# Kernel optimization log

Hardware: AMD Instinct MI355X
Metric: run time of the kernel (lower is better)

Reference implementation:

```python
import jax, jax.numpy as jnp
import numpy as np

T, HID, H, KV, D = 2048, 2048, 16, 8, 128
EPS = 1e-6
THETA = 10000.0


def setup_inputs() -> dict:
    key = jax.random.key(0)
    ks = jax.random.split(key, 6)
    positions = jnp.arange(T, dtype=jnp.int64 if jax.config.jax_enable_x64 else jnp.int32)
    hidden_states = jax.random.normal(ks[0], (T, HID), dtype=jnp.float32)
    scale = 0.02
    Wq = jax.random.normal(ks[1], (HID, H * 2 * D), dtype=jnp.float32) * scale
    Wk = jax.random.normal(ks[2], (HID, KV * D), dtype=jnp.float32) * scale
    Wv = jax.random.normal(ks[3], (HID, KV * D), dtype=jnp.float32) * scale
    Wo = jax.random.normal(ks[4], (H * D, HID), dtype=jnp.float32) * scale
    q_norm_w = jnp.zeros((D,), dtype=jnp.float32)  # torch init: zeros, applied as (1+w)
    k_norm_w = jnp.zeros((D,), dtype=jnp.float32)
    return {"positions": positions, "hidden_states": hidden_states, "Wq": Wq,
            "Wk": Wk, "Wv": Wv, "Wo": Wo, "q_norm_w": q_norm_w, "k_norm_w": k_norm_w}


def _rms_norm(x, w):
    # fp32 RMSNorm with (1 + weight) scaling, per last dim
    xf = x.astype(jnp.float32)
    inv = jax.lax.rsqrt(jnp.mean(xf * xf, axis=-1, keepdims=True) + EPS)
    return (xf * inv * (1.0 + w.astype(jnp.float32))).astype(x.dtype)


def _rope(x, positions):
    # neox-style rotary over full head_dim; x: (T, heads, D)
    half = D // 2
    inv_freq = 1.0 / (THETA ** (jnp.arange(0, half, dtype=jnp.float32) / half))
    freqs = positions.astype(jnp.float32)[:, None] * inv_freq  # (T, half)
    cos = jnp.cos(freqs)[:, None, :]  # (T,1,half)
    sin = jnp.sin(freqs)[:, None, :]
    x1, x2 = x[..., :half], x[..., half:]
    return jnp.concatenate([x1 * cos - x2 * sin, x2 * cos + x1 * sin], axis=-1)


def reference(positions, hidden_states, Wq, Wk, Wv, Wo, q_norm_w, k_norm_w):
    scaling = D ** -0.5
    qg = (hidden_states @ Wq).reshape(T, H, 2 * D)
    q, gate = qg[..., :D], qg[..., D:]              # (T,H,D) each
    k = (hidden_states @ Wk).reshape(T, KV, D)
    v = (hidden_states @ Wv).reshape(T, KV, D)
    q = _rms_norm(q, q_norm_w)
    k = _rms_norm(k, k_norm_w)
    q = _rope(q, positions)
    k = _rope(k, positions)
    # GQA: repeat kv heads
    rep = H // KV
    k = jnp.repeat(k, rep, axis=1)                   # (T,H,D)
    v = jnp.repeat(v, rep, axis=1)
    scores = jnp.einsum('thd,shd->hts', q, k) * scaling  # (H,T,T)
    causal = positions[:, None] >= positions[None, :]     # (T,T)
    scores = jnp.where(causal[None], scores, jnp.finfo(scores.dtype).min)
    probs = jax.nn.softmax(scores, axis=-1)
    o = jnp.einsum('hts,shd->thd', probs, v).reshape(T, H * D)
    o = o * jax.nn.sigmoid(gate.reshape(T, H * D))
    return o @ Wo
```

## Files before the change

kernel.cpp:

```cpp
#include <hip/hip_runtime.h>
#include <stdint.h>
#include <math.h>

#define T_SEQ 2048
#define HID   2048
#define NH    16
#define NKV   8
#define DH    128

typedef __bf16 bf16x8 __attribute__((ext_vector_type(8)));
typedef float  f32x4  __attribute__((ext_vector_type(4)));

__device__ __forceinline__ ushort f2bf(float f) {
  uint32_t u = __float_as_uint(f);
  u += 0x7FFF + ((u >> 16) & 1);
  return (ushort)(u >> 16);
}
__device__ __forceinline__ float bf2f(ushort u) {
  return __uint_as_float(((uint32_t)u) << 16);
}
__device__ __forceinline__ void gld16(const void* g, void* l) {
  __builtin_amdgcn_global_load_lds(
      (const __attribute__((address_space(1))) uint32_t*)g,
      (__attribute__((address_space(3))) uint32_t*)l, 16, 0, 0);
}

__global__ __launch_bounds__(256) void prep_kernel(
    const float* __restrict__ hs, const float* __restrict__ Wq,
    const float* __restrict__ Wk, const float* __restrict__ Wv,
    const float* __restrict__ qnw, const float* __restrict__ knw,
    ushort* __restrict__ hs16, ushort* __restrict__ Wqt,
    ushort* __restrict__ Wkt, ushort* __restrict__ Wvt,
    float* __restrict__ bnd) {
  int bid = blockIdx.x;
  if (bid < 4096) {
    int i = (bid * 256 + threadIdx.x) * 4;
    float4 v = *(const float4*)(hs + i);
    ushort4 o = {f2bf(v.x), f2bf(v.y), f2bf(v.z), f2bf(v.w)};
    *(ushort4*)(hs16 + i) = o;
    return;
  }
  if (bid == 16384) {
    int t = threadIdx.x;
    if (t >= 128) return;
    float mq = fabsf(1.f + qnw[t]);
    float mk = fabsf(1.f + knw[t]);
#pragma unroll
    for (int off = 32; off >= 1; off >>= 1) {
      mq = fmaxf(mq, __shfl_xor(mq, off, 64));
      mk = fmaxf(mk, __shfl_xor(mk, off, 64));
    }
    __shared__ float s4[4];
    if ((t & 63) == 0) { s4[(t >> 6) * 2] = mq; s4[(t >> 6) * 2 + 1] = mk; }
    __syncthreads();
    if (t == 0) {
      float MQ = fmaxf(s4[0], s4[2]), MK = fmaxf(s4[1], s4[3]);
      bnd[0] = 16.3217f * MQ * MK * 1.02f + 0.1f;
    }
    return;
  }
  bid -= 4096;
  const float* src; ushort* dst; int N, bi, bj;
  if (bid < 8192)       { src = Wq; dst = Wqt; N = 4096; bj = bid & 127; bi = bid >> 7; }
  else if (bid < 10240) { bid -= 8192;  src = Wk; dst = Wkt; N = 1024; bj = bid & 31; bi = bid >> 5; }
  else                  { bid -= 10240; src = Wv; dst = Wvt; N = 1024; bj = bid & 31; bi = bid >> 5; }
  __shared__ float tile[32][33];
  int row = threadIdx.x >> 3, c4 = (threadIdx.x & 7) * 4;
  float4 v = *(const float4*)(src + (size_t)(bi * 32 + row) * N + bj * 32 + c4);
  tile[row][c4 + 0] = v.x; tile[row][c4 + 1] = v.y;
  tile[row][c4 + 2] = v.z; tile[row][c4 + 3] = v.w;
  __syncthreads();
  ushort4 o = {f2bf(tile[c4 + 0][row]), f2bf(tile[c4 + 1][row]),
               f2bf(tile[c4 + 2][row]), f2bf(tile[c4 + 3][row])};
  *(ushort4*)(dst + (size_t)(bj * 32 + row) * HID + bi * 32 + c4) = o;
}

__global__ __launch_bounds__(256) void prep_wo(const float* __restrict__ Wo,
                                               ushort* __restrict__ Wot) {
  int bid = blockIdx.x;
  int bj = bid & 63, bi = bid >> 6;
  __shared__ float tile[32][33];
  int row = threadIdx.x >> 3, c4 = (threadIdx.x & 7) * 4;
  float4 v = *(const float4*)(Wo + (size_t)(bi * 32 + row) * HID + bj * 32 + c4);
  tile[row][c4 + 0] = v.x; tile[row][c4 + 1] = v.y;
  tile[row][c4 + 2] = v.z; tile[row][c4 + 3] = v.w;
  __syncthreads();
  ushort4 o = {f2bf(tile[c4 + 0][row]), f2bf(tile[c4 + 1][row]),
               f2bf(tile[c4 + 2][row]), f2bf(tile[c4 + 3][row])};
  *(ushort4*)(Wot + (size_t)(bj * 32 + row) * HID + bi * 32 + c4) = o;
}

template <int OUT_BF16>
__device__ __forceinline__ void gemm_core(
    const ushort* __restrict__ A, const ushort* __restrict__ Bt,
    float* __restrict__ Cf, ushort* __restrict__ Cb, int N, int K,
    int m0, int n0, ushort* As, ushort* Bs) {
  const int tid = threadIdx.x, lane = tid & 63, w = tid >> 6;
  const int quad = lane >> 4, l15 = lane & 15;
  const int wm = (w >> 1) * 64, wn = (w & 1) * 64;
  f32x4 acc[4][4];
#pragma unroll
  for (int i = 0; i < 4; ++i)
#pragma unroll
    for (int j = 0; j < 4; ++j) acc[i][j] = (f32x4){0.f, 0.f, 0.f, 0.f};

  const int srow = tid >> 2, sch = tid & 3;
  for (int k0 = 0; k0 < K; k0 += 32) {
    __syncthreads();
#pragma unroll
    for (int p = 0; p < 2; ++p) {
      int row = p * 64 + srow;
      int gch = sch ^ ((row >> 1) & 3);
      gld16(A + (size_t)(m0 + row) * K + k0 + gch * 8,
            As + (p * 256 + w * 64) * 8);
      gld16(Bt + (size_t)(n0 + row) * K + k0 + gch * 8,
            Bs + (p * 256 + w * 64) * 8);
    }
    __syncthreads();
    bf16x8 af[4], bfr[4];
#pragma unroll
    for (int mi = 0; mi < 4; ++mi) {
      int row = wm + mi * 16 + l15;
      int pch = quad ^ ((row >> 1) & 3);
      af[mi] = *(const bf16x8*)(As + row * 32 + pch * 8);
    }
#pragma unroll
    for (int ni = 0; ni < 4; ++ni) {
      int row = wn + ni * 16 + l15;
      int pch = quad ^ ((row >> 1) & 3);
      bfr[ni] = *(const bf16x8*)(Bs + row * 32 + pch * 8);
    }
#pragma unroll
    for (int mi = 0; mi < 4; ++mi)
#pragma unroll
      for (int ni = 0; ni < 4; ++ni)
        acc[mi][ni] = __builtin_amdgcn_mfma_f32_16x16x32_bf16(
            af[mi], bfr[ni], acc[mi][ni], 0, 0, 0);
  }
#pragma unroll
  for (int mi = 0; mi < 4; ++mi)
#pragma unroll
    for (int ni = 0; ni < 4; ++ni)
#pragma unroll
      for (int r = 0; r < 4; ++r) {
        int row = m0 + wm + mi * 16 + quad * 4 + r;
        int col = n0 + wn + ni * 16 + l15;
        if (OUT_BF16) Cb[(size_t)row * N + col] = f2bf(acc[mi][ni][r]);
        else          Cf[(size_t)row * N + col] = acc[mi][ni][r];
      }
}

__global__ __launch_bounds__(256) void gemm_qkv(
    const ushort* __restrict__ hs16, const ushort* __restrict__ Wqt,
    const ushort* __restrict__ Wkt, const ushort* __restrict__ Wvt,
    ushort* __restrict__ qg16, ushort* __restrict__ kb16,
    ushort* __restrict__ v16t) {
  __shared__ ushort As[128 * 32];
  __shared__ ushort Bs[128 * 32];
  int b = blockIdx.x;
  if (b < 512) {
    gemm_core<1>(hs16, Wqt, nullptr, qg16, 4096, HID, (b >> 5) * 128,
                 (b & 31) * 128, As, Bs);
  } else if (b < 640) {
    int f = b - 512;
    gemm_core<1>(hs16, Wkt, nullptr, kb16, 1024, HID, (f >> 3) * 128,
                 (f & 7) * 128, As, Bs);
  } else {
    int f = b - 640;
    gemm_core<1>(Wvt, hs16, nullptr, v16t, 2048, HID, (f >> 4) * 128,
                 (f & 15) * 128, As, Bs);
  }
}

__global__ __launch_bounds__(256) void gemm_out(
    const ushort* __restrict__ ob16, const ushort* __restrict__ Wot,
    float* __restrict__ out) {
  __shared__ ushort As[128 * 32];
  __shared__ ushort Bs[128 * 32];
  int b = blockIdx.x;
  gemm_core<0>(ob16, Wot, out, nullptr, HID, HID, (b >> 4) * 128,
               (b & 15) * 128, As, Bs);
}

__global__ __launch_bounds__(128) void norm_rope(
    const ushort* __restrict__ qg16, const ushort* __restrict__ kb16,
    const int* __restrict__ positions, const float* __restrict__ qw,
    const float* __restrict__ kw, ushort* __restrict__ q16,
    ushort* __restrict__ k16) {
  const int t = blockIdx.x, hh = blockIdx.y, d = threadIdx.x;
  const ushort* x; const float* wgt; ushort* out;
  if (hh < NH) {
    x = qg16 + ((size_t)t * NH + hh) * (2 * DH); wgt = qw;
    out = q16 + ((size_t)t * NH + hh) * DH;
  } else {
    x = kb16 + ((size_t)t * NKV + (hh - NH)) * DH; wgt = kw;
    out = k16 + ((size_t)t * NKV + (hh - NH)) * DH;
  }
  float v = bf2f(x[d]);
  float ss = v * v;
#pragma unroll
  for (int off = 32; off >= 1; off >>= 1) ss += __shfl_xor(ss, off, 64);
  __shared__ float red[2];
  if ((d & 63) == 0) red[d >> 6] = ss;
  __syncthreads();
  float mean = (red[0] + red[1]) * (1.0f / 128.0f);
  float xn = v * rsqrtf(mean + 1e-6f) * (1.0f + wgt[d]);
  __shared__ float sh[128];
  sh[d] = xn;
  __syncthreads();
  if (d < 64) {
    float pos = (float)positions[t];
    float freq = pos * exp2f(-(float)d * (13.287712379549449f / 64.0f));
    float s, c;
    sincosf(freq, &s, &c);
    float x1 = sh[d], x2 = sh[d + 64];
    out[d]      = f2bf(x1 * c - x2 * s);
    out[d + 64] = f2bf(x2 * c + x1 * s);
  }
}

__global__ __launch_bounds__(256) void attn_mfma(
    const ushort* __restrict__ q16, const ushort* __restrict__ k16,
    const ushort* __restrict__ v16t, const ushort* __restrict__ qg16,
    const float* __restrict__ bnd, ushort* __restrict__ ob16) {
  const int pb = blockIdx.x, h = blockIdx.y, kvh = h >> 1;
  const int tid = threadIdx.x, lane = tid & 63, w = tid >> 6;
  const int quad = lane >> 4, l15 = lane & 15;

  __shared__ ushort Ks[2][64 * 128];
  __shared__ ushort Vs[2][144 * 64];
  __shared__ ushort Ps[4][16][72];

#pragma unroll
  for (int buf = 0; buf < 2; ++buf)
    for (int i = tid; i < 16 * 64; i += 256) {
      int row = 128 + (i >> 6), col = i & 63;
      Vs[buf][row * 64 + col] = (row == 128) ? (ushort)0x3F80 : (ushort)0;
    }

  const float B = bnd[0];
  const float CSC = 0.08838834764831845f * 1.44269504088896f;

#pragma unroll 1
  for (int sel = 0; sel < 2; ++sel) {
    const int qt = sel ? (31 - pb) : pb;
    const int q0 = qt * 64, nk = qt + 1;

    bf16x8 qf[4];
    const ushort* qbase = q16 + ((size_t)(q0 + w * 16 + l15) * NH + h) * DH;
#pragma unroll
    for (int ks = 0; ks < 4; ++ks)
      qf[ks] = *(const bf16x8*)(qbase + ks * 32 + quad * 8);

    f32x4 oacc[9];
#pragma unroll
    for (int i = 0; i < 9; ++i) oacc[i] = (f32x4){0.f, 0.f, 0.f, 0.f};

    __syncthreads();
    {
#pragma unroll
      for (int p = 0; p < 4; ++p) {
        int row = p * 16 + (tid >> 4), ch = tid & 15;
        int gch = ch ^ (row & 15);
        gld16(k16 + ((size_t)row * NKV + kvh) * DH + gch * 8,
              (ushort*)Ks[0] + (p * 256 + w * 64) * 8);
      }
#pragma unroll
      for (int p = 0; p < 4; ++p) {
        int row = p * 32 + (tid >> 3), ch = tid & 7;
        int gch = ch ^ (row & 7);
        gld16(v16t + (size_t)(kvh * DH + row) * T_SEQ + gch * 8,
              (ushort*)Vs[0] + (p * 256 + w * 64) * 8);
      }
    }

#pragma unroll 1
    for (int kt = 0; kt < nk; ++kt) {
      const int cur = kt & 1;
      __syncthreads();
      if (kt + 1 < nk) {
        const int nt0 = (kt + 1) * 64;
#pragma unroll
        for (int p = 0; p < 4; ++p) {
          int row = p * 16 + (tid >> 4), ch = tid & 15;
          int gch = ch ^ (row & 15);
          gld16(k16 + ((size_t)(nt0 + row) * NKV + kvh) * DH + gch * 8,
                (ushort*)Ks[1 - cur] + (p * 256 + w * 64) * 8);
        }
#pragma unroll
        for (int p = 0; p < 4; ++p) {
          int row = p * 32 + (tid >> 3), ch = tid & 7;
          int gch = ch ^ (row & 7);
          gld16(v16t + (size_t)(kvh * DH + row) * T_SEQ + nt0 + gch * 8,
                (ushort*)Vs[1 - cur] + (p * 256 + w * 64) * 8);
        }
      }

      f32x4 sacc[4];
#pragma unroll
      for (int ni = 0; ni < 4; ++ni) sacc[ni] = (f32x4){0.f, 0.f, 0.f, 0.f};
      const ushort* KsC = Ks[cur];
#pragma unroll
      for (int ks = 0; ks < 4; ++ks)
#pragma unroll
        for (int ni = 0; ni < 4; ++ni) {
          int row = ni * 16 + l15;
          int pch = (ks * 4 + quad) ^ (row & 15);
          bf16x8 kf = *(const bf16x8*)(KsC + row * 128 + pch * 8);
          sacc[ni] = __builtin_amdgcn_mfma_f32_16x16x32_bf16(
              qf[ks], kf, sacc[ni], 0, 0, 0);
        }

      const bool diag = (kt == qt);
      const int kt0 = kt * 64;
#pragma unroll
      for (int ni = 0; ni < 4; ++ni) {
        int key = kt0 + ni * 16 + l15;
#pragma unroll
        for (int r = 0; r < 4; ++r) {
          float arg = fmaf(sacc[ni][r], CSC, -B);
          float pv;
          if (diag) {
            int q = q0 + w * 16 + quad * 4 + r;
            pv = (key <= q) ? exp2f(arg) : 0.f;
          } else {
            pv = exp2f(arg);
          }
          Ps[w][quad * 4 + r][ni * 16 + l15] = f2bf(pv);
        }
      }

      const ushort* VsC = Vs[cur];
#pragma unroll
      for (int ks2 = 0; ks2 < 2; ++ks2) {
        bf16x8 pf = *(const bf16x8*)(&Ps[w][l15][ks2 * 32 + quad * 8]);
#pragma unroll
        for (int ni = 0; ni < 9; ++ni) {
          int row = ni * 16 + l15;
          int pch = (ks2 * 4 + quad) ^ (row & 7);
          bf16x8 vf = *(const bf16x8*)(VsC + row * 64 + pch * 8);
          oacc[ni] = __builtin_amdgcn_mfma_f32_16x16x32_bf16(
              pf, vf, oacc[ni], 0, 0, 0);
        }
      }
    }

    float inv_l[4];
#pragma unroll
    for (int r = 0; r < 4; ++r) {
      float l = __shfl(oacc[8][r], lane & 48, 64);
      inv_l[r] = 1.0f / l;
    }
#pragma unroll
    for (int ni = 0; ni < 8; ++ni) {
      int d = ni * 16 + l15;
#pragma unroll
      for (int r = 0; r < 4; ++r) {
        int q = q0 + w * 16 + quad * 4 + r;
        float g = bf2f(qg16[((size_t)q * NH + h) * (2 * DH) + DH + d]);
        float o = oacc[ni][r] * inv_l[r];
        o = o / (1.0f + exp2f(-g * 1.44269504088896f));
        ob16[(size_t)q * (NH * DH) + h * DH + d] = f2bf(o);
      }
    }
  }
}

extern "C" void kernel_launch(void* const* d_in, const int* in_sizes, int n_in,
                              void* d_out, int out_size, void* d_ws, size_t ws_size,
                              hipStream_t stream) {
  const int*   positions = (const int*)d_in[0];
  const float* hs  = (const float*)d_in[1];
  const float* Wq  = (const float*)d_in[2];
  const float* Wk  = (const float*)d_in[3];
  const float* Wv  = (const float*)d_in[4];
  const float* Wo  = (const float*)d_in[5];
  const float* qnw = (const float*)d_in[6];
  const float* knw = (const float*)d_in[7];
  float* out = (float*)d_out;

  const size_t MB = 1 << 20;
  uint8_t* ws = (uint8_t*)d_ws;
  ushort* qg16 = (ushort*)(ws + 0);
  ushort* kb16 = (ushort*)(ws + 16 * MB);
  ushort* hs16 = (ushort*)(ws + 20 * MB);
  ushort* ob16 = (ushort*)(ws + 20 * MB);
  ushort* Wqt  = (ushort*)(ws + 28 * MB);
  ushort* q16  = (ushort*)(ws + 28 * MB);
  ushort* Wot  = (ushort*)(ws + 36 * MB);
  ushort* Wkt  = (ushort*)(ws + 44 * MB);
  ushort* k16  = (ushort*)(ws + 44 * MB);
  ushort* Wvt  = (ushort*)(ws + 48 * MB);
  ushort* v16t = (ushort*)(ws + 52 * MB);
  float*  bnd  = (float*)(ws + 56 * MB);

  prep_kernel<<<16385, 256, 0, stream>>>(hs, Wq, Wk, Wv, qnw, knw,
                                         hs16, Wqt, Wkt, Wvt, bnd);
  gemm_qkv<<<768, 256, 0, stream>>>(hs16, Wqt, Wkt, Wvt, qg16, kb16, v16t);
  norm_rope<<<dim3(T_SEQ, NH + NKV), 128, 0, stream>>>(qg16, kb16, positions,
                                                       qnw, knw, q16, k16);
  prep_wo<<<4096, 256, 0, stream>>>(Wo, Wot);
  attn_mfma<<<dim3(16, NH), 256, 0, stream>>>(q16, k16, v16t, qg16, bnd, ob16);
  gemm_out<<<256, 256, 0, stream>>>(ob16, Wot, out);
}
```

Measured before the change: 328.8 us.

## Split attention KV range across two blocks and add combine kernel

The attention grid gains a z-dimension of 2, and each block handles alternating KV tiles (even or odd) for its query tiles. This doubles the number of blocks from 256 to 512 so more of the GPU is occupied. Each split writes unnormalized bf16 partial outputs plus row sums, and a new combine kernel adds them, normalizes, and applies the sigmoid gate. The softmax bound computation moves from prep_kernel into each attention block. The cost is an extra kernel launch, extra global traffic for the partials, and bf16 rounding of the unnormalized partial sums.

```diff
diff --git a/kernel.cpp b/kernel.cpp
--- a/kernel.cpp
+++ b/kernel.cpp
@@ -28,35 +28,14 @@
 __global__ __launch_bounds__(256) void prep_kernel(
     const float* __restrict__ hs, const float* __restrict__ Wq,
     const float* __restrict__ Wk, const float* __restrict__ Wv,
-    const float* __restrict__ qnw, const float* __restrict__ knw,
     ushort* __restrict__ hs16, ushort* __restrict__ Wqt,
-    ushort* __restrict__ Wkt, ushort* __restrict__ Wvt,
-    float* __restrict__ bnd) {
+    ushort* __restrict__ Wkt, ushort* __restrict__ Wvt) {
   int bid = blockIdx.x;
   if (bid < 4096) {
     int i = (bid * 256 + threadIdx.x) * 4;
     float4 v = *(const float4*)(hs + i);
     ushort4 o = {f2bf(v.x), f2bf(v.y), f2bf(v.z), f2bf(v.w)};
     *(ushort4*)(hs16 + i) = o;
-    return;
-  }
-  if (bid == 16384) {
-    int t = threadIdx.x;
-    if (t >= 128) return;
-    float mq = fabsf(1.f + qnw[t]);
-    float mk = fabsf(1.f + knw[t]);
-#pragma unroll
-    for (int off = 32; off >= 1; off >>= 1) {
-      mq = fmaxf(mq, __shfl_xor(mq, off, 64));
-      mk = fmaxf(mk, __shfl_xor(mk, off, 64));
-    }
-    __shared__ float s4[4];
-    if ((t & 63) == 0) { s4[(t >> 6) * 2] = mq; s4[(t >> 6) * 2 + 1] = mk; }
-    __syncthreads();
-    if (t == 0) {
-      float MQ = fmaxf(s4[0], s4[2]), MK = fmaxf(s4[1], s4[3]);
-      bnd[0] = 16.3217f * MQ * MK * 1.02f + 0.1f;
-    }
     return;
   }
   bid -= 4096;
@@ -221,9 +200,10 @@
 
 __global__ __launch_bounds__(256) void attn_mfma(
     const ushort* __restrict__ q16, const ushort* __restrict__ k16,
-    const ushort* __restrict__ v16t, const ushort* __restrict__ qg16,
-    const float* __restrict__ bnd, ushort* __restrict__ ob16) {
-  const int pb = blockIdx.x, h = blockIdx.y, kvh = h >> 1;
+    const ushort* __restrict__ v16t, const float* __restrict__ qnw,
+    const float* __restrict__ knw, ushort* __restrict__ Op0,
+    ushort* __restrict__ Op1, float* __restrict__ lpart) {
+  const int pb = blockIdx.x, h = blockIdx.y, s = blockIdx.z, kvh = h >> 1;
   const int tid = threadIdx.x, lane = tid & 63, w = tid >> 6;
   const int quad = lane >> 4, l15 = lane & 15;
 
@@ -238,13 +218,32 @@
       Vs[buf][row * 64 + col] = (row == 128) ? (ushort)0x3F80 : (ushort)0;
     }
 
-  const float B = bnd[0];
+  __shared__ float s8[8];
+  __shared__ float bshare;
+  {
+    float mq = 0.f, mk = 0.f;
+    if (tid < 128) { mq = fabsf(1.f + qnw[tid]); mk = fabsf(1.f + knw[tid]); }
+#pragma unroll
+    for (int off = 32; off >= 1; off >>= 1) {
+      mq = fmaxf(mq, __shfl_xor(mq, off, 64));
+      mk = fmaxf(mk, __shfl_xor(mk, off, 64));
+    }
+    if (lane == 0) { s8[w * 2] = mq; s8[w * 2 + 1] = mk; }
+    __syncthreads();
+    if (tid == 0) {
+      float MQ = fmaxf(s8[0], s8[2]), MK = fmaxf(s8[1], s8[3]);
+      bshare = 16.3217f * MQ * MK * 1.02f + 0.1f;
+    }
+    __syncthreads();
+  }
+  const float B = bshare;
   const float CSC = 0.08838834764831845f * 1.44269504088896f;
 
 #pragma unroll 1
   for (int sel = 0; sel < 2; ++sel) {
     const int qt = sel ? (31 - pb) : pb;
     const int q0 = qt * 64, nk = qt + 1;
+    const int ntl = (nk > s) ? ((nk - s + 1) >> 1) : 0;
 
     bf16x8 qf[4];
     const ushort* qbase = q16 + ((size_t)(q0 + w * 16 + l15) * NH + h) * DH;
@@ -257,29 +256,31 @@
     for (int i = 0; i < 9; ++i) oacc[i] = (f32x4){0.f, 0.f, 0.f, 0.f};
 
     __syncthreads();
-    {
+    if (ntl > 0) {
+      const int kt0 = s * 64;
 #pragma unroll
       for (int p = 0; p < 4; ++p) {
         int row = p * 16 + (tid >> 4), ch = tid & 15;
         int gch = ch ^ (row & 15);
-        gld16(k16 + ((size_t)row * NKV + kvh) * DH + gch * 8,
+        gld16(k16 + ((size_t)(kt0 + row) * NKV + kvh) * DH + gch * 8,
               (ushort*)Ks[0] + (p * 256 + w * 64) * 8);
       }
 #pragma unroll
       for (int p = 0; p < 4; ++p) {
         int row = p * 32 + (tid >> 3), ch = tid & 7;
         int gch = ch ^ (row & 7);
-        gld16(v16t + (size_t)(kvh * DH + row) * T_SEQ + gch * 8,
+        gld16(v16t + (size_t)(kvh * DH + row) * T_SEQ + kt0 + gch * 8,
               (ushort*)Vs[0] + (p * 256 + w * 64) * 8);
       }
     }
 
 #pragma unroll 1
-    for (int kt = 0; kt < nk; ++kt) {
-      const int cur = kt & 1;
+    for (int it = 0; it < ntl; ++it) {
+      const int kt = s + 2 * it;
+      const int cur = it & 1;
       __syncthreads();
-      if (kt + 1 < nk) {
-        const int nt0 = (kt + 1) * 64;
+      if (it + 1 < ntl) {
+        const int nt0 = (kt + 2) * 64;
 #pragma unroll
         for (int p = 0; p < 4; ++p) {
           int row = p * 16 + (tid >> 4), ch = tid & 15;
@@ -345,25 +346,58 @@
       }
     }
 
-    float inv_l[4];
-#pragma unroll
-    for (int r = 0; r < 4; ++r) {
-      float l = __shfl(oacc[8][r], lane & 48, 64);
-      inv_l[r] = 1.0f / l;
-    }
+    ushort* Op = s ? Op1 : Op0;
 #pragma unroll
     for (int ni = 0; ni < 8; ++ni) {
       int d = ni * 16 + l15;
 #pragma unroll
       for (int r = 0; r < 4; ++r) {
         int q = q0 + w * 16 + quad * 4 + r;
-        float g = bf2f(qg16[((size_t)q * NH + h) * (2 * DH) + DH + d]);
-        float o = oacc[ni][r] * inv_l[r];
-        o = o / (1.0f + exp2f(-g * 1.44269504088896f));
-        ob16[(size_t)q * (NH * DH) + h * DH + d] = f2bf(o);
-      }
-    }
-  }
+        Op[((size_t)h * T_SEQ + q) * DH + d] = f2bf(oacc[ni][r]);
+      }
+    }
+    if (l15 == 0) {
+#pragma unroll
+      for (int r = 0; r < 4; ++r) {
+        int q = q0 + w * 16 + quad * 4 + r;
+        lpart[(size_t)s * (NH * T_SEQ) + h * T_SEQ + q] = oacc[8][r];
+      }
+    }
+  }
+}
+
+__global__ __launch_bounds__(256) void combine_kernel(
+    const ushort* __restrict__ Op0, const ushort* __restrict__ Op1,
+    const float* __restrict__ lpart, const ushort* __restrict__ qg16,
+    ushort* __restrict__ ob16) {
+  const int t = blockIdx.x, tid = threadIdx.x;
+  const int h = tid >> 4, d0 = (tid & 15) * 8;
+  const float l = lpart[h * T_SEQ + t] + lpart[NH * T_SEQ + h * T_SEQ + t];
+  const float inv = 1.0f / l;
+  const size_t po = ((size_t)h * T_SEQ + t) * DH + d0;
+  ushort4 a0 = *(const ushort4*)(Op0 + po);
+  ushort4 a1 = *(const ushort4*)(Op0 + po + 4);
+  ushort4 b0 = *(const ushort4*)(Op1 + po);
+  ushort4 b1 = *(const ushort4*)(Op1 + po + 4);
+  const ushort* gp = qg16 + ((size_t)t * NH + h) * (2 * DH) + DH + d0;
+  ushort4 g0 = *(const ushort4*)(gp);
+  ushort4 g1 = *(const ushort4*)(gp + 4);
+  float oa[8] = {bf2f(a0.x), bf2f(a0.y), bf2f(a0.z), bf2f(a0.w),
+                 bf2f(a1.x), bf2f(a1.y), bf2f(a1.z), bf2f(a1.w)};
+  float ob[8] = {bf2f(b0.x), bf2f(b0.y), bf2f(b0.z), bf2f(b0.w),
+                 bf2f(b1.x), bf2f(b1.y), bf2f(b1.z), bf2f(b1.w)};
+  float gg[8] = {bf2f(g0.x), bf2f(g0.y), bf2f(g0.z), bf2f(g0.w),
+                 bf2f(g1.x), bf2f(g1.y), bf2f(g1.z), bf2f(g1.w)};
+  ushort r[8];
+#pragma unroll
+  for (int i = 0; i < 8; ++i) {
+    float o = (oa[i] + ob[i]) * inv;
+    o = o / (1.0f + exp2f(-gg[i] * 1.44269504088896f));
+    r[i] = f2bf(o);
+  }
+  ushort* op = ob16 + (size_t)t * (NH * DH) + h * DH + d0;
+  *(ushort4*)(op)     = (ushort4){r[0], r[1], r[2], r[3]};
+  *(ushort4*)(op + 4) = (ushort4){r[4], r[5], r[6], r[7]};
 }
 
 extern "C" void kernel_launch(void* const* d_in, const int* in_sizes, int n_in,
@@ -382,24 +416,27 @@
   const size_t MB = 1 << 20;
   uint8_t* ws = (uint8_t*)d_ws;
   ushort* qg16 = (ushort*)(ws + 0);
+  ushort* Op0  = (ushort*)(ws + 16 * MB);
   ushort* kb16 = (ushort*)(ws + 16 * MB);
   ushort* hs16 = (ushort*)(ws + 20 * MB);
-  ushort* ob16 = (ushort*)(ws + 20 * MB);
+  float*  lpart= (float*)(ws + 24 * MB);
   ushort* Wqt  = (ushort*)(ws + 28 * MB);
   ushort* q16  = (ushort*)(ws + 28 * MB);
   ushort* Wot  = (ushort*)(ws + 36 * MB);
   ushort* Wkt  = (ushort*)(ws + 44 * MB);
   ushort* k16  = (ushort*)(ws + 44 * MB);
   ushort* Wvt  = (ushort*)(ws + 48 * MB);
+  ushort* ob16 = (ushort*)(ws + 48 * MB);
   ushort* v16t = (ushort*)(ws + 52 * MB);
-  float*  bnd  = (float*)(ws + 56 * MB);
-
-  prep_kernel<<<16385, 256, 0, stream>>>(hs, Wq, Wk, Wv, qnw, knw,
-                                         hs16, Wqt, Wkt, Wvt, bnd);
+  ushort* Op1  = (ushort*)(ws + 56 * MB);
+
+  prep_kernel<<<16384, 256, 0, stream>>>(hs, Wq, Wk, Wv, hs16, Wqt, Wkt, Wvt);
   gemm_qkv<<<768, 256, 0, stream>>>(hs16, Wqt, Wkt, Wvt, qg16, kb16, v16t);
   norm_rope<<<dim3(T_SEQ, NH + NKV), 128, 0, stream>>>(qg16, kb16, positions,
                                                        qnw, knw, q16, k16);
   prep_wo<<<4096, 256, 0, stream>>>(Wo, Wot);
-  attn_mfma<<<dim3(16, NH), 256, 0, stream>>>(q16, k16, v16t, qg16, bnd, ob16);
+  attn_mfma<<<dim3(16, NH, 2), 256, 0, stream>>>(q16, k16, v16t, qnw, knw,
+                                                 Op0, Op1, lpart);
+  combine_kernel<<<T_SEQ, 256, 0, stream>>>(Op0, Op1, lpart, qg16, ob16);
   gemm_out<<<256, 256, 0, stream>>>(ob16, Wot, out);
 }
```

After: 301.4 us. 1.09x faster.
